# Kernel optimization log

Measured on AMD Instinct MI355X. Metric: run time of the kernel, lower is better.

The kernel has to match this reference:

```python
import jax, jax.numpy as jnp
import numpy as np

B, S = 4096, 4096
NS, FDIM = 16, 64


def _ln(x, g, b):
    mu = jnp.mean(x, axis=-1, keepdims=True)
    v = jnp.mean((x - mu) ** 2, axis=-1, keepdims=True)
    return (x - mu) / jnp.sqrt(v + 1e-5) * g + b


def _rolling_vol_mean(returns, w):
    # mean over all length-w windows of unbiased std (matches per-window torch.std loop)
    Bn, L = returns.shape
    z = jnp.zeros((Bn, 1), returns.dtype)
    c1 = jnp.concatenate([z, jnp.cumsum(returns, axis=1)], axis=1)
    c2 = jnp.concatenate([z, jnp.cumsum(returns * returns, axis=1)], axis=1)
    s = c1[:, w:] - c1[:, :-w]    # [B, L-w+1] window sums
    s2 = c2[:, w:] - c2[:, :-w]
    var = (s2 - s * s / w) / (w - 1)
    return jnp.mean(jnp.sqrt(jnp.maximum(var, 0.0)), axis=1, keepdims=True)


def setup_inputs() -> dict:
    key = jax.random.key(0)
    ks = jax.random.split(key, 24)
    r = lambda i, shp: jax.random.normal(ks[i], shp, jnp.float32) * 0.05
    return {
        'price_series': jax.random.uniform(ks[0], (B, S, 1), jnp.float32) * 10.0 + 1.0,
        're_W': r(1, (4, 4, 64)), 're_b': r(2, (4, 64)),
        're_g': jnp.ones((4, 64), jnp.float32), 're_beta': jnp.zeros((4, 64), jnp.float32),
        'rh_W1': r(3, (256, 64)), 'rh_b1': r(4, (64,)), 'rh_W2': r(5, (64, 4)), 'rh_b2': r(6, (4,)),
        'rv_W': r(7, (3, 128)), 'rv_b': r(8, (128,)),
        'rv_g': jnp.ones((128,), jnp.float32), 'rv_beta': jnp.zeros((128,), jnp.float32),
        'vs_W': r(9, (128, 128)), 'vs_b': r(10, (128,)),
        'vs_g': jnp.ones((128,), jnp.float32), 'vs_beta': jnp.zeros((128,), jnp.float32),
        'vc_W1': r(11, (256, 64)), 'vc_b1': r(12, (64,)), 'vc_W2': r(13, (64, 4)), 'vc_b2': r(14, (4,)),
        'emb': r(15, (NS, FDIM)),
        'cn_W1': r(16, (576, 128)), 'cn_b1': r(17, (128,)),
        'cn_W2': r(18, (128, 64)), 'cn_b2': r(19, (64,)),
        'cn_W3': r(20, (64, 1)), 'cn_b3': r(21, (1,)),
    }


def reference(price_series, re_W, re_b, re_g, re_beta, rh_W1, rh_b1, rh_W2, rh_b2,
              rv_W, rv_b, rv_g, rv_beta, vs_W, vs_b, vs_g, vs_beta,
              vc_W1, vc_b1, vc_W2, vc_b2, emb, cn_W1, cn_b1, cn_W2, cn_b2, cn_W3, cn_b3):
    prices = price_series[:, :, 0]            # [B,S]
    Bn, Sn = prices.shape
    # --- MarketRegimeEncoder: SMA-20 via prefix sums (the per-step torch loop) ---
    cs = jnp.cumsum(prices, axis=1)
    shifted = jnp.concatenate([jnp.zeros((Bn, 20), prices.dtype), cs[:, :-20]], axis=1)
    counts = jnp.minimum(jnp.arange(Sn) + 1, 20).astype(prices.dtype)
    sma20 = (cs - shifted) / counts           # (sma_5 is computed but unused in original)
    trend = jnp.mean((prices - sma20) / (sma20 + 1e-8), axis=1, keepdims=True)
    p10 = prices[:, Sn - 10:Sn - 9]
    momentum = (prices[:, -1:] - p10) / (p10 + 1e-8)
    pmean = jnp.mean(prices, axis=1, keepdims=True)
    mean_rev = (prices[:, -1:] - pmean) / (pmean + 1e-8)
    pstd = jnp.std(prices, axis=1, keepdims=True, ddof=1)
    cycle = pstd / (pmean + 1e-8)
    combined = jnp.concatenate([trend, momentum, mean_rev, cycle], axis=1)  # [B,4]
    h = jax.nn.relu(jnp.einsum('bi,kio->bko', combined, re_W) + re_b[None])  # [B,4,64]
    h = _ln(h, re_g[None], re_beta[None])
    regime_features = h.reshape(Bn, -1)        # [B,256] (trend|momentum|mean_rev|cycle)
    logits = jax.nn.relu(regime_features @ rh_W1 + rh_b1) @ rh_W2 + rh_b2
    regime_probs = jax.nn.softmax(logits, axis=1)
    # --- VolatilityEncodingModule ---
    logp = jnp.log(jnp.maximum(price_series, 1e-8))
    returns = jnp.diff(logp, axis=1)[:, :, 0]  # [B,S-1]
    vol_in = jnp.concatenate([_rolling_vol_mean(returns, w) for w in (5, 10, 20)], axis=1)  # [B,3]
    rv = _ln(jax.nn.relu(vol_in @ rv_W + rv_b), rv_g, rv_beta)
    vs = _ln(jax.nn.relu(rv @ vs_W + vs_b), vs_g, vs_beta)
    vol_features = jnp.concatenate([rv, vs], axis=1)  # [B,256]
    vlogits = jax.nn.relu(vol_features @ vc_W1 + vc_b1) @ vc_W2 + vc_b2
    vol_regime = jax.nn.softmax(vlogits, axis=1)
    # --- OptionsStrategyEncoder: vectorized over strategies ---
    mv = jnp.concatenate([regime_features, vol_features], axis=1)  # [B,512]
    mvp = mv @ cn_W1[:512]                    # [B,128]
    ep = emb @ cn_W1[512:]                    # [NS,128]
    h1 = jax.nn.relu(mvp[:, None, :] + ep[None, :, :] + cn_b1)  # [B,NS,128]
    h2 = jax.nn.relu(h1 @ cn_W2 + cn_b2)      # [B,NS,64]
    scores = (h2 @ cn_W3 + cn_b3)[:, :, 0]    # [B,NS]
    return regime_features, regime_probs, vol_features, vol_regime, scores
```

## Files before the change

### kernel.cpp

```cpp
#include <hip/hip_runtime.h>
#include <math.h>

#define NROWS 4096
#define SLEN  4096
#define RETN  4095
#define STRD  274

__global__ __launch_bounds__(256) void k_ep(const float* __restrict__ emb,
                                            const float* __restrict__ cn_W1,
                                            const float* __restrict__ cn_b1,
                                            float* __restrict__ ep) {
    int idx = blockIdx.x * 256 + threadIdx.x;
    if (idx >= 16 * 128) return;
    int n = idx >> 7, o = idx & 127;
    float acc = cn_b1[o];
    const float* w = cn_W1 + 512 * 128;
    for (int i = 0; i < 64; ++i) acc = fmaf(emb[n * 64 + i], w[i * 128 + o], acc);
    ep[idx] = acc;
}

__global__ __launch_bounds__(256, 4) void k_stats(const float* __restrict__ price,
                                                  float* __restrict__ combined,
                                                  float* __restrict__ volin) {
    __shared__ float scm[16 * STRD];
    __shared__ float red[6][4];

    const int tid = threadIdx.x;
    const int row = blockIdx.x;
    const float* pr = price + (size_t)row * SLEN;

    float pA = 0.f, pB = 0.f;
    if (tid == 0) { pA = pr[SLEN - 10]; pB = pr[SLEN - 1]; }

    if (tid < 32) scm[(tid & 15) * STRD + (tid >> 4)] = 0.f;
    scm[(tid & 15) * STRD + 258 + (tid >> 4)] = 0.f;

    #pragma unroll
    for (int it = 0; it < 4; ++it) {
        const int i = it * 256 + tid;
        const float4 v = ((const float4*)pr)[i];
        const int base = (4 * (i & 3)) * STRD + (i >> 2) + 2;
        scm[base]            = v.x;
        scm[base + STRD]     = v.y;
        scm[base + 2 * STRD] = v.z;
        scm[base + 3 * STRD] = v.w;
    }
    __syncthreads();

    const int s0 = tid * 16;

    float hb[20];
    #pragma unroll
    for (int k = 0; k < 20; ++k)
        hb[k] = (k < 4) ? scm[(12 + k) * STRD + tid]
                        : scm[(k - 4) * STRD + (tid + 1)];
    float x_[16];
    #pragma unroll
    for (int d = 0; d < 16; ++d) x_[d] = scm[d * STRD + (tid + 2)];

    float W = 0.f;
    #pragma unroll
    for (int k = 0; k < 20; ++k) W += hb[k];
    float st = 0.f, s1p = 0.f, s2p = 0.f;
    #pragma unroll
    for (int d = 0; d < 16; ++d) {
        const float x = x_[d];
        W += x - hb[d];
        float inv_cnt = 0.05f;
        if (s0 == 0)                 inv_cnt = 1.0f / (float)(d + 1);
        else if (s0 == 16 && d < 3)  inv_cnt = 1.0f / (float)(17 + d);
        const float sma = W * inv_cnt;
        st  = fmaf(x - sma, __builtin_amdgcn_rcpf(sma + 1e-8f), st);
        s1p += x;
        s2p = fmaf(x, x, s2p);
    }

    float lg[17];
    #pragma unroll
    for (int d = 0; d < 16; ++d) lg[d] = __builtin_amdgcn_logf(fmaxf(x_[d], 1e-8f));
    lg[16] = __builtin_amdgcn_logf(fmaxf(scm[0 * STRD + (tid + 3)], 1e-8f));
    float rs[20];
    #pragma unroll
    for (int d = 0; d < 16; ++d) rs[d] = lg[d + 1] - lg[d];

    __syncthreads();

    #pragma unroll
    for (int d = 0; d < 16; ++d)
        if (s0 + d < RETN) scm[d * STRD + (tid + 2)] = rs[d];
    __syncthreads();

    #pragma unroll
    for (int j = 0; j < 4; ++j) rs[16 + j] = scm[j * STRD + (tid + 3)];

    float S5 = 0.f, Q5 = 0.f, S10 = 0.f, Q10 = 0.f, S20 = 0.f, Q20 = 0.f;
    #pragma unroll
    for (int j = 0; j < 20; ++j) {
        const float x = rs[j];
        S20 += x; Q20 = fmaf(x, x, Q20);
        if (j < 10) { S10 += x; Q10 = fmaf(x, x, Q10); }
        if (j < 5)  { S5  += x; Q5  = fmaf(x, x, Q5); }
    }

    #define SQT(S, Q, invw, invw1) \
        __builtin_amdgcn_sqrtf(fmaxf(fmaf(-(S) * (invw), (S), (Q)) * (invw1), 0.f))
    #define X5(d)  ((d) < 15 ? rs[(d) + 5]  : scm[4 * STRD + (tid + 3)])
    #define X10(d) ((d) < 10 ? rs[(d) + 10] : scm[((d) - 6) * STRD + (tid + 3)])
    #define X20(d) ((d) < 12 ? scm[((d) + 4) * STRD + (tid + 3)] \
                             : scm[((d) - 12) * STRD + (tid + 4)])

    float v5 = 0.f, v10 = 0.f, v20 = 0.f;
    if (tid < 254) {
        #pragma unroll
        for (int d = 0; d < 16; ++d) {
            v5  += SQT(S5,  Q5,  0.2f,  0.25f);
            v10 += SQT(S10, Q10, 0.1f,  1.f / 9.f);
            v20 += SQT(S20, Q20, 0.05f, 1.f / 19.f);
            const float xo = rs[d], qo = xo * xo;
            const float a5 = X5(d), a10 = X10(d), a20 = X20(d);
            S5  += a5  - xo;  Q5  = fmaf(a5,  a5,  Q5)  - qo;
            S10 += a10 - xo;  Q10 = fmaf(a10, a10, Q10) - qo;
            S20 += a20 - xo;  Q20 = fmaf(a20, a20, Q20) - qo;
        }
    } else {
        #pragma unroll
        for (int d = 0; d < 16; ++d) {
            const int i = s0 + d;
            if (i < 4091) v5  += SQT(S5,  Q5,  0.2f,  0.25f);
            if (i < 4086) v10 += SQT(S10, Q10, 0.1f,  1.f / 9.f);
            if (i < 4076) v20 += SQT(S20, Q20, 0.05f, 1.f / 19.f);
            const float xo = rs[d], qo = xo * xo;
            const float a5 = X5(d), a10 = X10(d), a20 = X20(d);
            S5  += a5  - xo;  Q5  = fmaf(a5,  a5,  Q5)  - qo;
            S10 += a10 - xo;  Q10 = fmaf(a10, a10, Q10) - qo;
            S20 += a20 - xo;  Q20 = fmaf(a20, a20, Q20) - qo;
        }
    }
    #undef SQT
    #undef X5
    #undef X10
    #undef X20

    {
        float vals[6] = {s1p, s2p, st, v5, v10, v20};
        const int lane = tid & 63, wid = tid >> 6;
        #pragma unroll
        for (int v = 0; v < 6; ++v) {
            float x = vals[v];
            for (int o = 32; o > 0; o >>= 1) x += __shfl_xor(x, o, 64);
            if (lane == 0) red[v][wid] = x;
        }
    }
    __syncthreads();
    if (tid == 0) {
        const float sum_p  = red[0][0] + red[0][1] + red[0][2] + red[0][3];
        const float sum_p2 = red[1][0] + red[1][1] + red[1][2] + red[1][3];
        const float sum_t  = red[2][0] + red[2][1] + red[2][2] + red[2][3];
        const float sv5    = red[3][0] + red[3][1] + red[3][2] + red[3][3];
        const float sv10   = red[4][0] + red[4][1] + red[4][2] + red[4][3];
        const float sv20   = red[5][0] + red[5][1] + red[5][2] + red[5][3];
        const float pmean = sum_p * (1.f / 4096.f);
        const float varp  = fmaf(-sum_p * (1.f / 4096.f), sum_p, sum_p2) * (1.f / 4095.f);
        const float pstd  = __builtin_amdgcn_sqrtf(fmaxf(varp, 0.f));
        const float ipm   = __builtin_amdgcn_rcpf(pmean + 1e-8f);
        combined[row * 4 + 0] = sum_t * (1.f / 4096.f);
        combined[row * 4 + 1] = (pB - pA) * __builtin_amdgcn_rcpf(pA + 1e-8f);
        combined[row * 4 + 2] = (pB - pmean) * ipm;
        combined[row * 4 + 3] = pstd * ipm;
        const float LN2 = 0.6931471805599453f;
        volin[row * 3 + 0] = sv5  * (LN2 / 4091.f);
        volin[row * 3 + 1] = sv10 * (LN2 / 4086.f);
        volin[row * 3 + 2] = sv20 * (LN2 / 4076.f);
    }
}

__global__ __launch_bounds__(256) void k_mlp(const float* __restrict__ combined,
                                             const float* __restrict__ volin,
                                             const float* __restrict__ re_W,  const float* __restrict__ re_b,
                                             const float* __restrict__ re_g,  const float* __restrict__ re_be,
                                             const float* __restrict__ rh_W1, const float* __restrict__ rh_b1,
                                             const float* __restrict__ rh_W2, const float* __restrict__ rh_b2,
                                             const float* __restrict__ rv_W,  const float* __restrict__ rv_b,
                                             const float* __restrict__ rv_g,  const float* __restrict__ rv_be,
                                             const float* __restrict__ vs_W,  const float* __restrict__ vs_b,
                                             const float* __restrict__ vs_g,  const float* __restrict__ vs_be,
                                             const float* __restrict__ vc_W1, const float* __restrict__ vc_b1,
                                             const float* __restrict__ vc_W2, const float* __restrict__ vc_b2,
                                             float* __restrict__ out_rf, float* __restrict__ out_rp,
                                             float* __restrict__ out_vf, float* __restrict__ out_vr) {
    __shared__ float rf_lds[8][256];
    __shared__ float vf_lds[8][256];
    __shared__ float ps[4][8][64];
    __shared__ float hid_s[8][64];
    __shared__ float prt[4][8];
    __shared__ float cmb_s[8][4];
    __shared__ float vol_s[8][3];

    const int tid  = threadIdx.x;
    const int lane = tid & 63;
    const int wid  = tid >> 6;
    const int row0 = blockIdx.x * 8;

    if (tid < 32) cmb_s[tid >> 2][tid & 3] = combined[(size_t)(row0 + (tid >> 2)) * 4 + (tid & 3)];
    else if (tid < 56) { int t = tid - 32; vol_s[t / 3][t % 3] = volin[(size_t)(row0 + t / 3) * 3 + t % 3]; }
    __syncthreads();

    {
        const float* w = re_W + wid * 256;
        const float w0 = w[lane], w1 = w[64 + lane], w2 = w[128 + lane], w3 = w[192 + lane];
        const float b  = re_b[wid * 64 + lane];
        const float gg = re_g[wid * 64 + lane], bb = re_be[wid * 64 + lane];
        float h[8], sm[8], sq[8];
        #pragma unroll
        for (int r = 0; r < 8; ++r) {
            float v = fmaf(cmb_s[r][0], w0, fmaf(cmb_s[r][1], w1,
                      fmaf(cmb_s[r][2], w2, fmaf(cmb_s[r][3], w3, b))));
            h[r] = fmaxf(v, 0.f);
            sm[r] = h[r]; sq[r] = h[r] * h[r];
        }
        #pragma unroll
        for (int off = 32; off > 0; off >>= 1) {
            #pragma unroll
            for (int r = 0; r < 8; ++r) {
                sm[r] += __shfl_xor(sm[r], off, 64);
                sq[r] += __shfl_xor(sq[r], off, 64);
            }
        }
        #pragma unroll
        for (int r = 0; r < 8; ++r) {
            const float mu  = sm[r] * (1.f / 64.f);
            const float var = fmaxf(sq[r] * (1.f / 64.f) - mu * mu, 0.f);
            const float y = (h[r] - mu) * rsqrtf(var + 1e-5f) * gg + bb;
            rf_lds[r][wid * 64 + lane] = y;
            out_rf[(size_t)(row0 + r) * 256 + wid * 64 + lane] = y;
        }
    }
    __syncthreads();

    {
        const int i0 = wid * 64;
        float acc[8] = {0.f, 0.f, 0.f, 0.f, 0.f, 0.f, 0.f, 0.f};
        for (int i = 0; i < 64; ++i) {
            const float wv = rh_W1[(size_t)(i0 + i) * 64 + lane];
            #pragma unroll
            for (int r = 0; r < 8; ++r) acc[r] = fmaf(rf_lds[r][i0 + i], wv, acc[r]);
        }
        #pragma unroll
        for (int r = 0; r < 8; ++r) ps[wid][r][lane] = acc[r];
    }
    __syncthreads();

    for (int it = tid; it < 512; it += 256) {
        const int r = it >> 6, o = it & 63;
        const float v = ps[0][r][o] + ps[1][r][o] + ps[2][r][o] + ps[3][r][o] + rh_b1[o];
        hid_s[r][o] = fmaxf(v, 0.f);
    }
    __syncthreads();

    if (tid < 32) {
        const int r = tid >> 2, j = tid & 3;
        float acc = rh_b2[j];
        for (int i = 0; i < 64; ++i) acc = fmaf(hid_s[r][i], rh_W2[i * 4 + j], acc);
        float m = acc;
        m = fmaxf(m, __shfl_xor(m, 1, 64));
        m = fmaxf(m, __shfl_xor(m, 2, 64));
        const float e = expf(acc - m);
        float s = e;
        s += __shfl_xor(s, 1, 64);
        s += __shfl_xor(s, 2, 64);
        out_rp[(size_t)(row0 + r) * 4 + j] = e / s;
    }

    {
        const int o = tid & 127, g = tid >> 7, wv_ = tid >> 6;
        const float w0 = rv_W[o], w1 = rv_W[128 + o], w2 = rv_W[256 + o];
        const float b = rv_b[o], gg = rv_g[o], bb = rv_be[o];
        float h[4], sm[4], sq[4];
        #pragma unroll
        for (int r4 = 0; r4 < 4; ++r4) {
            const int r = g * 4 + r4;
            float v = fmaf(vol_s[r][0], w0, fmaf(vol_s[r][1], w1, fmaf(vol_s[r][2], w2, b)));
            h[r4] = fmaxf(v, 0.f);
            sm[r4] = h[r4]; sq[r4] = h[r4] * h[r4];
        }
        #pragma unroll
        for (int off = 32; off > 0; off >>= 1) {
            #pragma unroll
            for (int r4 = 0; r4 < 4; ++r4) {
                sm[r4] += __shfl_xor(sm[r4], off, 64);
                sq[r4] += __shfl_xor(sq[r4], off, 64);
            }
        }
        if (lane == 0) {
            #pragma unroll
            for (int r4 = 0; r4 < 4; ++r4) { prt[wv_][r4 * 2] = sm[r4]; prt[wv_][r4 * 2 + 1] = sq[r4]; }
        }
        __syncthreads();
        #pragma unroll
        for (int r4 = 0; r4 < 4; ++r4) {
            const float S = prt[2 * g][2 * r4]     + prt[2 * g + 1][2 * r4];
            const float Q = prt[2 * g][2 * r4 + 1] + prt[2 * g + 1][2 * r4 + 1];
            const float mu  = S * (1.f / 128.f);
            const float var = fmaxf(Q * (1.f / 128.f) - mu * mu, 0.f);
            const float y = (h[r4] - mu) * rsqrtf(var + 1e-5f) * gg + bb;
            vf_lds[g * 4 + r4][o] = y;
            out_vf[(size_t)(row0 + g * 4 + r4) * 256 + o] = y;
        }
    }
    __syncthreads();

    {
        const int o = tid & 127, g = tid >> 7, wv_ = tid >> 6;
        float acc[4];
        const float b = vs_b[o];
        #pragma unroll
        for (int r4 = 0; r4 < 4; ++r4) acc[r4] = b;
        for (int i = 0; i < 128; ++i) {
            const float wv = vs_W[(size_t)i * 128 + o];
            #pragma unroll
            for (int r4 = 0; r4 < 4; ++r4) acc[r4] = fmaf(vf_lds[g * 4 + r4][i], wv, acc[r4]);
        }
        const float gg = vs_g[o], bb = vs_be[o];
        float h[4], sm[4], sq[4];
        #pragma unroll
        for (int r4 = 0; r4 < 4; ++r4) {
            h[r4] = fmaxf(acc[r4], 0.f);
            sm[r4] = h[r4]; sq[r4] = h[r4] * h[r4];
        }
        #pragma unroll
        for (int off = 32; off > 0; off >>= 1) {
            #pragma unroll
            for (int r4 = 0; r4 < 4; ++r4) {
                sm[r4] += __shfl_xor(sm[r4], off, 64);
                sq[r4] += __shfl_xor(sq[r4], off, 64);
            }
        }
        __syncthreads();
        if (lane == 0) {
            #pragma unroll
            for (int r4 = 0; r4 < 4; ++r4) { prt[wv_][r4 * 2] = sm[r4]; prt[wv_][r4 * 2 + 1] = sq[r4]; }
        }
        __syncthreads();
        #pragma unroll
        for (int r4 = 0; r4 < 4; ++r4) {
            const float S = prt[2 * g][2 * r4]     + prt[2 * g + 1][2 * r4];
            const float Q = prt[2 * g][2 * r4 + 1] + prt[2 * g + 1][2 * r4 + 1];
            const float mu  = S * (1.f / 128.f);
            const float var = fmaxf(Q * (1.f / 128.f) - mu * mu, 0.f);
            const float y = (h[r4] - mu) * rsqrtf(var + 1e-5f) * gg + bb;
            vf_lds[g * 4 + r4][128 + o] = y;
            out_vf[(size_t)(row0 + g * 4 + r4) * 256 + 128 + o] = y;
        }
    }
    __syncthreads();

    {
        const int i0 = wid * 64;
        float acc[8] = {0.f, 0.f, 0.f, 0.f, 0.f, 0.f, 0.f, 0.f};
        for (int i = 0; i < 64; ++i) {
            const float wv = vc_W1[(size_t)(i0 + i) * 64 + lane];
            #pragma unroll
            for (int r = 0; r < 8; ++r) acc[r] = fmaf(vf_lds[r][i0 + i], wv, acc[r]);
        }
        #pragma unroll
        for (int r = 0; r < 8; ++r) ps[wid][r][lane] = acc[r];
    }
    __syncthreads();

    for (int it = tid; it < 512; it += 256) {
        const int r = it >> 6, o = it & 63;
        const float v = ps[0][r][o] + ps[1][r][o] + ps[2][r][o] + ps[3][r][o] + vc_b1[o];
        hid_s[r][o] = fmaxf(v, 0.f);
    }
    __syncthreads();
    if (tid < 32) {
        const int r = tid >> 2, j = tid & 3;
        float acc = vc_b2[j];
        for (int i = 0; i < 64; ++i) acc = fmaf(hid_s[r][i], vc_W2[i * 4 + j], acc);
        float m = acc;
        m = fmaxf(m, __shfl_xor(m, 1, 64));
        m = fmaxf(m, __shfl_xor(m, 2, 64));
        const float e = expf(acc - m);
        float s = e;
        s += __shfl_xor(s, 1, 64);
        s += __shfl_xor(s, 2, 64);
        out_vr[(size_t)(row0 + r) * 4 + j] = e / s;
    }
}

__global__ __launch_bounds__(512, 4) void k_cross(const float* __restrict__ rfin,
                                                  const float* __restrict__ vfin,
                                                  const float* __restrict__ cn_W1,
                                                  const float* __restrict__ cn_W2,
                                                  const float* __restrict__ cn_b2,
                                                  const float* __restrict__ cn_W3,
                                                  const float* __restrict__ cn_b3,
                                                  const float* __restrict__ ep,
                                                  float* __restrict__ scores) {
    __shared__ __align__(16) float w2s[128 * 64];
    __shared__ __align__(16) float uni[4096];
    __shared__ __align__(16) float mvs[4][512];
    __shared__ __align__(16) float mvp_s[4][128];
    __shared__ __align__(16) float epb[16][132];

    const int tid  = threadIdx.x;
    const int lane = tid & 63;
    const int wv   = tid >> 6;
    const int row0 = blockIdx.x * 4;

    {
        const int r = tid >> 7, cq = tid & 127;
        const float* src = (cq < 64)
            ? (rfin + (size_t)(row0 + r) * 256 + 4 * cq)
            : (vfin + (size_t)(row0 + r) * 256 + 4 * (cq - 64));
        *(float4*)&mvs[r][4 * cq] = *(const float4*)src;
    }
    #pragma unroll
    for (int k = 0; k < 4; ++k) {
        const int idx = k * 512 + tid;
        *(float4*)&w2s[4 * idx] = *(const float4*)(cn_W2 + 4 * idx);
    }
    {
        const int ns = tid >> 5, c4 = (tid & 31) * 4;
        *(float4*)&epb[ns][c4] = *(const float4*)(ep + ns * 128 + c4);
    }
    __syncthreads();

    {
        const int p = lane >> 5;
        const int q = lane & 31;
        float acc[4][4] = {{0.f}};
        const int ibase = wv * 64 + p;
        #pragma unroll 8
        for (int s = 0; s < 32; ++s) {
            const int i = ibase + 2 * s;
            const float4 w1v = *(const float4*)(cn_W1 + (size_t)i * 128 + 4 * q);
            const float m0 = mvs[0][i], m1 = mvs[1][i], m2 = mvs[2][i], m3 = mvs[3][i];
            acc[0][0] = fmaf(m0, w1v.x, acc[0][0]); acc[0][1] = fmaf(m0, w1v.y, acc[0][1]);
            acc[0][2] = fmaf(m0, w1v.z, acc[0][2]); acc[0][3] = fmaf(m0, w1v.w, acc[0][3]);
            acc[1][0] = fmaf(m1, w1v.x, acc[1][0]); acc[1][1] = fmaf(m1, w1v.y, acc[1][1]);
            acc[1][2] = fmaf(m1, w1v.z, acc[1][2]); acc[1][3] = fmaf(m1, w1v.w, acc[1][3]);
            acc[2][0] = fmaf(m2, w1v.x, acc[2][0]); acc[2][1] = fmaf(m2, w1v.y, acc[2][1]);
            acc[2][2] = fmaf(m2, w1v.z, acc[2][2]); acc[2][3] = fmaf(m2, w1v.w, acc[2][3]);
            acc[3][0] = fmaf(m3, w1v.x, acc[3][0]); acc[3][1] = fmaf(m3, w1v.y, acc[3][1]);
            acc[3][2] = fmaf(m3, w1v.z, acc[3][2]); acc[3][3] = fmaf(m3, w1v.w, acc[3][3]);
        }
        #pragma unroll
        for (int r = 0; r < 4; ++r) {
            #pragma unroll
            for (int k = 0; k < 4; ++k) acc[r][k] += __shfl_xor(acc[r][k], 32, 64);
        }
        if (p == 0) {
            #pragma unroll
            for (int r = 0; r < 4; ++r)
                *(float4*)&uni[wv * 512 + r * 128 + 4 * q] =
                    make_float4(acc[r][0], acc[r][1], acc[r][2], acc[r][3]);
        }
    }
    __syncthreads();

    {
        const int r = tid >> 7, c = tid & 127;
        float s = 0.f;
        #pragma unroll
        for (int w = 0; w < 8; ++w) s += uni[w * 512 + r * 128 + c];
        mvp_s[r][c] = s;
    }
    __syncthreads();

    const int ch  = tid >> 8;
    const int nst = tid & 255;
    const int ns  = nst >> 4;
    const int t   = nst & 15;
    float acc[4][4];
    #pragma unroll
    for (int r = 0; r < 4; ++r)
        #pragma unroll
        for (int k = 0; k < 4; ++k) acc[r][k] = 0.f;
    {
        const int c0 = ch * 64;
        #pragma unroll 2
        for (int cb = 0; cb < 64; cb += 4) {
            const int c = c0 + cb;
            float4 m4[4];
            #pragma unroll
            for (int r = 0; r < 4; ++r) m4[r] = *(const float4*)&mvp_s[r][c];
            const float4 e4 = *(const float4*)&epb[ns][c];
            {   const float4 w2v = *(const float4*)&w2s[(c + 0) * 64 + 4 * t];
                #pragma unroll
                for (int r = 0; r < 4; ++r) {
                    const float h = fmaxf(m4[r].x + e4.x, 0.f);
                    acc[r][0] = fmaf(h, w2v.x, acc[r][0]); acc[r][1] = fmaf(h, w2v.y, acc[r][1]);
                    acc[r][2] = fmaf(h, w2v.z, acc[r][2]); acc[r][3] = fmaf(h, w2v.w, acc[r][3]); } }
            {   const float4 w2v = *(const float4*)&w2s[(c + 1) * 64 + 4 * t];
                #pragma unroll
                for (int r = 0; r < 4; ++r) {
                    const float h = fmaxf(m4[r].y + e4.y, 0.f);
                    acc[r][0] = fmaf(h, w2v.x, acc[r][0]); acc[r][1] = fmaf(h, w2v.y, acc[r][1]);
                    acc[r][2] = fmaf(h, w2v.z, acc[r][2]); acc[r][3] = fmaf(h, w2v.w, acc[r][3]); } }
            {   const float4 w2v = *(const float4*)&w2s[(c + 2) * 64 + 4 * t];
                #pragma unroll
                for (int r = 0; r < 4; ++r) {
                    const float h = fmaxf(m4[r].z + e4.z, 0.f);
                    acc[r][0] = fmaf(h, w2v.x, acc[r][0]); acc[r][1] = fmaf(h, w2v.y, acc[r][1]);
                    acc[r][2] = fmaf(h, w2v.z, acc[r][2]); acc[r][3] = fmaf(h, w2v.w, acc[r][3]); } }
            {   const float4 w2v = *(const float4*)&w2s[(c + 3) * 64 + 4 * t];
                #pragma unroll
                for (int r = 0; r < 4; ++r) {
                    const float h = fmaxf(m4[r].w + e4.w, 0.f);
                    acc[r][0] = fmaf(h, w2v.x, acc[r][0]); acc[r][1] = fmaf(h, w2v.y, acc[r][1]);
                    acc[r][2] = fmaf(h, w2v.z, acc[r][2]); acc[r][3] = fmaf(h, w2v.w, acc[r][3]); } }
        }
    }
    __syncthreads();
    if (ch == 1) {
        #pragma unroll
        for (int r = 0; r < 4; ++r)
            *(float4*)&uni[nst * 16 + r * 4] = make_float4(acc[r][0], acc[r][1], acc[r][2], acc[r][3]);
    }
    __syncthreads();
    if (ch == 0) {
        #pragma unroll
        for (int r = 0; r < 4; ++r) {
            const float4 o = *(const float4*)&uni[nst * 16 + r * 4];
            acc[r][0] += o.x; acc[r][1] += o.y; acc[r][2] += o.z; acc[r][3] += o.w;
        }
        const float4 b2v = *(const float4*)(cn_b2 + 4 * t);
        const float4 w3v = *(const float4*)(cn_W3 + 4 * t);
        const float  b3v = cn_b3[0];
        #pragma unroll
        for (int r = 0; r < 4; ++r) {
            float s =      fmaxf(acc[r][0] + b2v.x, 0.f) * w3v.x;
            s = fmaf(fmaxf(acc[r][1] + b2v.y, 0.f), w3v.y, s);
            s = fmaf(fmaxf(acc[r][2] + b2v.z, 0.f), w3v.z, s);
            s = fmaf(fmaxf(acc[r][3] + b2v.w, 0.f), w3v.w, s);
            s += __shfl_xor(s, 1, 64);
            s += __shfl_xor(s, 2, 64);
            s += __shfl_xor(s, 4, 64);
            s += __shfl_xor(s, 8, 64);
            if (t == 0) scores[(size_t)(row0 + r) * 16 + ns] = s + b3v;
        }
    }
}

extern "C" void kernel_launch(void* const* d_in, const int* in_sizes, int n_in,
                              void* d_out, int out_size, void* d_ws, size_t ws_size,
                              hipStream_t stream) {
    (void)in_sizes; (void)n_in; (void)out_size; (void)ws_size;

    const float* price = (const float*)d_in[0];
    const float* re_W  = (const float*)d_in[1];
    const float* re_b  = (const float*)d_in[2];
    const float* re_g  = (const float*)d_in[3];
    const float* re_be = (const float*)d_in[4];
    const float* rh_W1 = (const float*)d_in[5];
    const float* rh_b1 = (const float*)d_in[6];
    const float* rh_W2 = (const float*)d_in[7];
    const float* rh_b2 = (const float*)d_in[8];
    const float* rv_W  = (const float*)d_in[9];
    const float* rv_b  = (const float*)d_in[10];
    const float* rv_g  = (const float*)d_in[11];
    const float* rv_be = (const float*)d_in[12];
    const float* vs_W  = (const float*)d_in[13];
    const float* vs_b  = (const float*)d_in[14];
    const float* vs_g  = (const float*)d_in[15];
    const float* vs_be = (const float*)d_in[16];
    const float* vc_W1 = (const float*)d_in[17];
    const float* vc_b1 = (const float*)d_in[18];
    const float* vc_W2 = (const float*)d_in[19];
    const float* vc_b2 = (const float*)d_in[20];
    const float* emb   = (const float*)d_in[21];
    const float* cn_W1 = (const float*)d_in[22];
    const float* cn_b1 = (const float*)d_in[23];
    const float* cn_W2 = (const float*)d_in[24];
    const float* cn_b2 = (const float*)d_in[25];
    const float* cn_W3 = (const float*)d_in[26];
    const float* cn_b3 = (const float*)d_in[27];

    float* out    = (float*)d_out;
    float* out_rf = out;
    float* out_rp = out_rf + 4096 * 256;
    float* out_vf = out_rp + 4096 * 4;
    float* out_vr = out_vf + 4096 * 256;
    float* out_sc = out_vr + 4096 * 4;

    float* ws       = (float*)d_ws;
    float* combined = ws;
    float* volin    = combined + 4096 * 4;
    float* ep       = volin + 4096 * 3;

    hipLaunchKernelGGL(k_ep,    dim3(8),    dim3(256), 0, stream, emb, cn_W1, cn_b1, ep);
    hipLaunchKernelGGL(k_stats, dim3(4096), dim3(256), 0, stream, price, combined, volin);
    hipLaunchKernelGGL(k_mlp,   dim3(512),  dim3(256), 0, stream, combined, volin,
                       re_W, re_b, re_g, re_be, rh_W1, rh_b1, rh_W2, rh_b2,
                       rv_W, rv_b, rv_g, rv_be, vs_W, vs_b, vs_g, vs_be,
                       vc_W1, vc_b1, vc_W2, vc_b2,
                       out_rf, out_rp, out_vf, out_vr);
    hipLaunchKernelGGL(k_cross, dim3(1024), dim3(512), 0, stream, out_rf, out_vf,
                       cn_W1, cn_W2, cn_b2, cn_W3, cn_b3, ep, out_sc);
}
```

Baseline: 100.6 us.

## Switch stats LDS to row-chunked layout with vector loads, hoist sqrt scaling

The k_stats shared-memory buffer changes from a column-strided layout (stride 274) to per-thread 20-float chunks. Global-to-LDS stores, window reads and the return-series exchange can then use float4 accesses, and each thread pulls all needed neighbour returns into registers (rs[36]) up front. That removes the per-element scalar LDS reads inside the rolling-window loop. The 1/(w-1) factor inside each sqrt moves out into the final constant as sqrt(1/(w-1)), which saves one multiply per window evaluation. The __launch_bounds__ occupancy hint is dropped, and the 80-byte row stride may cause some LDS bank conflicts on the 128-bit accesses.

```diff
diff --git a/kernel.cpp b/kernel.cpp
--- a/kernel.cpp
+++ b/kernel.cpp
@@ -4,7 +4,7 @@
 #define NROWS 4096
 #define SLEN  4096
 #define RETN  4095
-#define STRD  274
+#define CHK   20
 
 __global__ __launch_bounds__(256) void k_ep(const float* __restrict__ emb,
                                             const float* __restrict__ cn_W1,
@@ -19,10 +19,10 @@
     ep[idx] = acc;
 }
 
-__global__ __launch_bounds__(256, 4) void k_stats(const float* __restrict__ price,
-                                                  float* __restrict__ combined,
-                                                  float* __restrict__ volin) {
-    __shared__ float scm[16 * STRD];
+__global__ void k_stats(const float* __restrict__ price,
+                        float* __restrict__ combined,
+                        float* __restrict__ volin) {
+    __shared__ float scm[260 * CHK];
     __shared__ float red[6][4];
 
     const int tid = threadIdx.x;
@@ -32,31 +32,27 @@
     float pA = 0.f, pB = 0.f;
     if (tid == 0) { pA = pr[SLEN - 10]; pB = pr[SLEN - 1]; }
 
-    if (tid < 32) scm[(tid & 15) * STRD + (tid >> 4)] = 0.f;
-    scm[(tid & 15) * STRD + 258 + (tid >> 4)] = 0.f;
+    if (tid < 40) { scm[tid] = 0.f; scm[258 * CHK + tid] = 0.f; }
 
     #pragma unroll
     for (int it = 0; it < 4; ++it) {
         const int i = it * 256 + tid;
         const float4 v = ((const float4*)pr)[i];
-        const int base = (4 * (i & 3)) * STRD + (i >> 2) + 2;
-        scm[base]            = v.x;
-        scm[base + STRD]     = v.y;
-        scm[base + 2 * STRD] = v.z;
-        scm[base + 3 * STRD] = v.w;
+        *(float4*)&scm[(2 + (i >> 2)) * CHK + ((4 * i) & 15)] = v;
     }
     __syncthreads();
 
     const int s0 = tid * 16;
 
-    float hb[20];
-    #pragma unroll
-    for (int k = 0; k < 20; ++k)
-        hb[k] = (k < 4) ? scm[(12 + k) * STRD + tid]
-                        : scm[(k - 4) * STRD + (tid + 1)];
-    float x_[16];
-    #pragma unroll
-    for (int d = 0; d < 16; ++d) x_[d] = scm[d * STRD + (tid + 2)];
+    float hb[20], x_[16];
+    *(float4*)&hb[0] = *(const float4*)&scm[tid * CHK + 12];
+    #pragma unroll
+    for (int k = 0; k < 4; ++k)
+        *(float4*)&hb[4 + 4 * k] = *(const float4*)&scm[(tid + 1) * CHK + 4 * k];
+    #pragma unroll
+    for (int k = 0; k < 4; ++k)
+        *(float4*)&x_[4 * k] = *(const float4*)&scm[(tid + 2) * CHK + 4 * k];
+    const float pn = scm[(tid + 3) * CHK];
 
     float W = 0.f;
     #pragma unroll
@@ -78,20 +74,21 @@
     float lg[17];
     #pragma unroll
     for (int d = 0; d < 16; ++d) lg[d] = __builtin_amdgcn_logf(fmaxf(x_[d], 1e-8f));
-    lg[16] = __builtin_amdgcn_logf(fmaxf(scm[0 * STRD + (tid + 3)], 1e-8f));
-    float rs[20];
+    lg[16] = __builtin_amdgcn_logf(fmaxf(pn, 1e-8f));
+    float rs[36];
     #pragma unroll
     for (int d = 0; d < 16; ++d) rs[d] = lg[d + 1] - lg[d];
 
     __syncthreads();
-
-    #pragma unroll
-    for (int d = 0; d < 16; ++d)
-        if (s0 + d < RETN) scm[d * STRD + (tid + 2)] = rs[d];
-    __syncthreads();
-
-    #pragma unroll
-    for (int j = 0; j < 4; ++j) rs[16 + j] = scm[j * STRD + (tid + 3)];
+    #pragma unroll
+    for (int k = 0; k < 4; ++k)
+        *(float4*)&scm[(tid + 2) * CHK + 4 * k] = *(const float4*)&rs[4 * k];
+    __syncthreads();
+
+    #pragma unroll
+    for (int k = 0; k < 4; ++k)
+        *(float4*)&rs[16 + 4 * k] = *(const float4*)&scm[(tid + 3) * CHK + 4 * k];
+    *(float4*)&rs[32] = *(const float4*)&scm[(tid + 4) * CHK];
 
     float S5 = 0.f, Q5 = 0.f, S10 = 0.f, Q10 = 0.f, S20 = 0.f, Q20 = 0.f;
     #pragma unroll
@@ -102,22 +99,18 @@
         if (j < 5)  { S5  += x; Q5  = fmaf(x, x, Q5); }
     }
 
-    #define SQT(S, Q, invw, invw1) \
-        __builtin_amdgcn_sqrtf(fmaxf(fmaf(-(S) * (invw), (S), (Q)) * (invw1), 0.f))
-    #define X5(d)  ((d) < 15 ? rs[(d) + 5]  : scm[4 * STRD + (tid + 3)])
-    #define X10(d) ((d) < 10 ? rs[(d) + 10] : scm[((d) - 6) * STRD + (tid + 3)])
-    #define X20(d) ((d) < 12 ? scm[((d) + 4) * STRD + (tid + 3)] \
-                             : scm[((d) - 12) * STRD + (tid + 4)])
+    #define SQT(S, Q, invw) \
+        __builtin_amdgcn_sqrtf(fmaxf(fmaf(-(S) * (invw), (S), (Q)), 0.f))
 
     float v5 = 0.f, v10 = 0.f, v20 = 0.f;
     if (tid < 254) {
         #pragma unroll
         for (int d = 0; d < 16; ++d) {
-            v5  += SQT(S5,  Q5,  0.2f,  0.25f);
-            v10 += SQT(S10, Q10, 0.1f,  1.f / 9.f);
-            v20 += SQT(S20, Q20, 0.05f, 1.f / 19.f);
+            v5  += SQT(S5,  Q5,  0.2f);
+            v10 += SQT(S10, Q10, 0.1f);
+            v20 += SQT(S20, Q20, 0.05f);
             const float xo = rs[d], qo = xo * xo;
-            const float a5 = X5(d), a10 = X10(d), a20 = X20(d);
+            const float a5 = rs[d + 5], a10 = rs[d + 10], a20 = rs[d + 20];
             S5  += a5  - xo;  Q5  = fmaf(a5,  a5,  Q5)  - qo;
             S10 += a10 - xo;  Q10 = fmaf(a10, a10, Q10) - qo;
             S20 += a20 - xo;  Q20 = fmaf(a20, a20, Q20) - qo;
@@ -126,20 +119,17 @@
         #pragma unroll
         for (int d = 0; d < 16; ++d) {
             const int i = s0 + d;
-            if (i < 4091) v5  += SQT(S5,  Q5,  0.2f,  0.25f);
-            if (i < 4086) v10 += SQT(S10, Q10, 0.1f,  1.f / 9.f);
-            if (i < 4076) v20 += SQT(S20, Q20, 0.05f, 1.f / 19.f);
+            if (i < 4091) v5  += SQT(S5,  Q5,  0.2f);
+            if (i < 4086) v10 += SQT(S10, Q10, 0.1f);
+            if (i < 4076) v20 += SQT(S20, Q20, 0.05f);
             const float xo = rs[d], qo = xo * xo;
-            const float a5 = X5(d), a10 = X10(d), a20 = X20(d);
+            const float a5 = rs[d + 5], a10 = rs[d + 10], a20 = rs[d + 20];
             S5  += a5  - xo;  Q5  = fmaf(a5,  a5,  Q5)  - qo;
             S10 += a10 - xo;  Q10 = fmaf(a10, a10, Q10) - qo;
             S20 += a20 - xo;  Q20 = fmaf(a20, a20, Q20) - qo;
         }
     }
     #undef SQT
-    #undef X5
-    #undef X10
-    #undef X20
 
     {
         float vals[6] = {s1p, s2p, st, v5, v10, v20};
@@ -168,9 +158,9 @@
         combined[row * 4 + 2] = (pB - pmean) * ipm;
         combined[row * 4 + 3] = pstd * ipm;
         const float LN2 = 0.6931471805599453f;
-        volin[row * 3 + 0] = sv5  * (LN2 / 4091.f);
-        volin[row * 3 + 1] = sv10 * (LN2 / 4086.f);
-        volin[row * 3 + 2] = sv20 * (LN2 / 4076.f);
+        volin[row * 3 + 0] = sv5  * (LN2 * 0.5f                 / 4091.f);
+        volin[row * 3 + 1] = sv10 * (LN2 * (1.f / 3.f)          / 4086.f);
+        volin[row * 3 + 2] = sv20 * (LN2 * 0.22941573387056174f / 4076.f);
     }
 }
 
```

After: 101.2 us. About the same (+0.5%).
